# Optimization experiments

Measured on AMD Instinct MI355X. Metric: run time of the kernel, lower is better.

Reference implementation:

```python
import jax, jax.numpy as jnp
import numpy as np

N, L, D = 8, 2048, 128


def setup_inputs() -> dict:
    key = jax.random.key(0)
    k1, k2, k3, k4 = jax.random.split(key, 4)
    x_t = jax.random.normal(k1, (N, L, D), jnp.float32)
    x_f = jax.random.normal(k2, (N, L, D), jnp.float32)
    W = jax.random.normal(k3, (D, D), jnp.float32) / np.sqrt(D)  # proj weight (torch Linear layout)
    b = jax.random.normal(k4, (D,), jnp.float32) * 0.02
    return {"x_t": x_t, "x_f": x_f, "W": W, "b": b}


def _col_score(a, c, scale):
    # softmax attention with zeroed diagonal, then column-sum -> [N, L]
    att = jnp.einsum('nld,nmd->nlm', a, c) * scale
    att = jax.nn.softmax(att, axis=-1)
    att = att * (1.0 - jnp.eye(att.shape[-1], dtype=att.dtype))
    return jnp.sum(att, axis=1)


def _mask(score, time):
    # score: [N, L]; k-th extreme threshold, k = L//2
    k = int(0.5 * score.shape[1])
    if time:
        vals, _ = jax.lax.top_k(score, k)          # k largest, descending
        theta = vals[:, -1:]                        # k-th largest
        return score > theta
    else:
        vals, _ = jax.lax.top_k(-score, k)          # k smallest
        theta = -vals[:, -1:]                       # k-th smallest
        return score <= theta


def reference(x_t, x_f, W, b):
    scale = 1.0 / np.sqrt(W.shape[0])
    pt = x_t @ W.T + b
    pf = x_f @ W.T + b
    score_t = _col_score(pt, pt, scale)
    score_f = _col_score(pf, pf, scale)
    score_tf = _col_score(pt, pf, scale)
    score_ft = _col_score(pf, pt, scale)
    mask_t = _mask(score_t, False)
    mask_f = _mask(score_f, False)
    mask_tf = _mask(score_tf, True)   # computed in original forward (unused in blend)
    mask_ft = _mask(score_ft, True)
    mask_t1 = (mask_t & ~mask_f)[:, :, None]   # [N, L, 1] broadcast over D
    mask_f1 = (mask_f & ~mask_t)[:, :, None]
    x_t1 = jnp.where(mask_t1, x_f, x_t)
    x_f1 = jnp.where(mask_f1, x_t, x_f)
    return (0.5 * (x_t1 + x_t), 0.5 * (x_f1 + x_f))
```

## Files before the change

kernel.cpp:

```cpp
#include <hip/hip_runtime.h>
#include <math.h>

#define LL 2048
#define DD 128
#define NS 16
#define SLAB (LL * DD)
#define SCALE 0.08838834764831845f
#define NT 16
#define NPAIR 136
#define LSTR 40

typedef __attribute__((ext_vector_type(8))) short short8v;
typedef __attribute__((ext_vector_type(4))) float float4v;

__device__ __forceinline__ unsigned int f2bf(float f) {
    unsigned int u = __float_as_uint(f);
    u += 0x7fffu + ((u >> 16) & 1u);
    return u >> 16;
}
__device__ __forceinline__ void pair_decode(int p, int& ib, int& jb) {
    int i = 0;
    while (p >= NT - i) { p -= NT - i; ++i; }
    ib = i; jb = i + p;
}

__global__ __launch_bounds__(256, 4) void proj_kernel(
    const float* __restrict__ xt, const float* __restrict__ xf,
    const float* __restrict__ W,  const float* __restrict__ bias,
    unsigned short* __restrict__ Ph, unsigned short* __restrict__ Pl)
{
    __shared__ float Alds[64 * 36];
    __shared__ float Blds[128 * 36];
    __shared__ float bs[128];
    const int ns = blockIdx.y;
    const int l0 = blockIdx.x * 64;
    const int src = ns >> 3, n = ns & 7;
    const float* x = (src ? xf : xt) + (size_t)n * LL * DD;
    const int tid = threadIdx.x;
    const int ty = tid >> 4, tx = tid & 15;

    if (tid < 128) bs[tid] = bias[tid];
    __syncthreads();

    float acc[4][8];
#pragma unroll
    for (int i = 0; i < 4; ++i)
#pragma unroll
        for (int j = 0; j < 8; ++j) acc[i][j] = bs[tx + 16 * j];

    for (int kc = 0; kc < 4; ++kc) {
        __syncthreads();
#pragma unroll
        for (int t = 0; t < 2; ++t) {
            int idx = tid + t * 256;
            int r = idx >> 3, k4 = (idx & 7) << 2;
            *(float4*)&Alds[r * 36 + k4] =
                *(const float4*)&x[(size_t)(l0 + r) * DD + kc * 32 + k4];
        }
#pragma unroll
        for (int t = 0; t < 4; ++t) {
            int idx = tid + t * 256;
            int r = idx >> 3, k4 = (idx & 7) << 2;
            *(float4*)&Blds[r * 36 + k4] =
                *(const float4*)&W[(size_t)r * DD + kc * 32 + k4];
        }
        __syncthreads();
#pragma unroll
        for (int k4 = 0; k4 < 32; k4 += 4) {
            float4 a4[4], b4[8];
#pragma unroll
            for (int i = 0; i < 4; ++i) a4[i] = *(const float4*)&Alds[(ty + 16 * i) * 36 + k4];
#pragma unroll
            for (int j = 0; j < 8; ++j) b4[j] = *(const float4*)&Blds[(tx + 16 * j) * 36 + k4];
#pragma unroll
            for (int i = 0; i < 4; ++i)
#pragma unroll
                for (int j = 0; j < 8; ++j) {
                    acc[i][j] = fmaf(a4[i].x, b4[j].x, acc[i][j]);
                    acc[i][j] = fmaf(a4[i].y, b4[j].y, acc[i][j]);
                    acc[i][j] = fmaf(a4[i].z, b4[j].z, acc[i][j]);
                    acc[i][j] = fmaf(a4[i].w, b4[j].w, acc[i][j]);
                }
        }
    }
#pragma unroll
    for (int i = 0; i < 4; ++i) {
        const size_t rowo = (size_t)ns * SLAB + (size_t)(l0 + ty + 16 * i) * DD;
#pragma unroll
        for (int j = 0; j < 8; ++j) {
            float p = acc[i][j];
            unsigned int hb = f2bf(p);
            float hf = __uint_as_float(hb << 16);
            unsigned int lb = f2bf(p - hf);
            Ph[rowo + tx + 16 * j] = (unsigned short)hb;
            Pl[rowo + tx + 16 * j] = (unsigned short)lb;
        }
    }
}

__device__ __forceinline__ void mfma_core(
    const unsigned short* __restrict__ Ph, const unsigned short* __restrict__ Pl,
    int ns, int ib, int jb, int tid,
    unsigned short* Ah, unsigned short* Alo, unsigned short* Bh, unsigned short* Blo,
    float4v acc[2][8])
{
    const int lane = tid & 63;
    const int quad = lane >> 4, l16 = lane & 15;
    const int wave = tid >> 6;
    const int arow = wave * 32;
    const unsigned short* sAh = Ph + (size_t)ns * SLAB + (size_t)ib * 128 * DD;
    const unsigned short* sAl = Pl + (size_t)ns * SLAB + (size_t)ib * 128 * DD;
    const unsigned short* sBh = Ph + (size_t)ns * SLAB + (size_t)jb * 128 * DD;
    const unsigned short* sBl = Pl + (size_t)ns * SLAB + (size_t)jb * 128 * DD;

#pragma unroll
    for (int rt = 0; rt < 2; ++rt)
#pragma unroll
        for (int ct = 0; ct < 8; ++ct)
#pragma unroll
            for (int r = 0; r < 4; ++r) acc[rt][ct][r] = 0.f;

    for (int kc = 0; kc < 4; ++kc) {
        __syncthreads();
#pragma unroll
        for (int it = 0; it < 2; ++it) {
            int idx = tid + it * 256;
            int r = idx >> 2, c4 = idx & 3;
            size_t go = (size_t)r * DD + kc * 32 + c4 * 8;
            int lo = r * LSTR + c4 * 8;
            *(uint4*)&Ah[lo]  = *(const uint4*)&sAh[go];
            *(uint4*)&Alo[lo] = *(const uint4*)&sAl[go];
            *(uint4*)&Bh[lo]  = *(const uint4*)&sBh[go];
            *(uint4*)&Blo[lo] = *(const uint4*)&sBl[go];
        }
        __syncthreads();
        const int kb = quad * 8;
        short8v bh[8], bl[8];
#pragma unroll
        for (int ct = 0; ct < 8; ++ct) {
            int ba = (ct * 16 + l16) * LSTR + kb;
            bh[ct] = *(const short8v*)&Bh[ba];
            bl[ct] = *(const short8v*)&Blo[ba];
        }
#pragma unroll
        for (int rt = 0; rt < 2; ++rt) {
            int aa = (arow + rt * 16 + l16) * LSTR + kb;
            short8v ah = *(const short8v*)&Ah[aa];
            short8v al = *(const short8v*)&Alo[aa];
#pragma unroll
            for (int ct = 0; ct < 8; ++ct) {
                acc[rt][ct] = __builtin_amdgcn_mfma_f32_16x16x32_bf16(ah, bh[ct], acc[rt][ct], 0, 0, 0);
                acc[rt][ct] = __builtin_amdgcn_mfma_f32_16x16x32_bf16(ah, bl[ct], acc[rt][ct], 0, 0, 0);
                acc[rt][ct] = __builtin_amdgcn_mfma_f32_16x16x32_bf16(al, bh[ct], acc[rt][ct], 0, 0, 0);
            }
        }
    }
}

__global__ __launch_bounds__(256, 3) void stats_kernel(
    const unsigned short* __restrict__ Ph, const unsigned short* __restrict__ Pl,
    float* __restrict__ Zpart)
{
    __shared__ unsigned int AhU[2560], AlU[2560], BhU[2560], BlU[2560];
    int ib, jb;  pair_decode(blockIdx.x, ib, jb);
    const int ns = blockIdx.y;
    const int tid = threadIdx.x;
    const int lane = tid & 63, quad = lane >> 4, l16 = lane & 15, wave = tid >> 6;
    const int arow = wave * 32;

    float4v acc[2][8];
    mfma_core(Ph, Pl, ns, ib, jb, tid,
              (unsigned short*)AhU, (unsigned short*)AlU,
              (unsigned short*)BhU, (unsigned short*)BlU, acc);

    float cs[8];
#pragma unroll
    for (int ct = 0; ct < 8; ++ct) cs[ct] = 0.f;

#pragma unroll
    for (int rt = 0; rt < 2; ++rt)
#pragma unroll
        for (int rg = 0; rg < 4; ++rg) {
            float e[8];
#pragma unroll
            for (int ct = 0; ct < 8; ++ct) e[ct] = __expf(acc[rt][ct][rg] * SCALE);
            float s = 0.f;
#pragma unroll
            for (int ct = 0; ct < 8; ++ct) { s += e[ct]; cs[ct] += e[ct]; }
            s += __shfl_xor(s, 1);
            s += __shfl_xor(s, 2);
            s += __shfl_xor(s, 4);
            s += __shfl_xor(s, 8);
            if (l16 == 0) {
                int o = (ns * 16 + jb) * LL + ib * 128 + arow + rt * 16 + quad * 4 + rg;
                Zpart[o] = s;
            }
        }

    if (ib != jb) {
#pragma unroll
        for (int ct = 0; ct < 8; ++ct) {
            float s = cs[ct];
            s += __shfl_xor(s, 16);
            s += __shfl_xor(s, 32);
            cs[ct] = s;
        }
        __syncthreads();
        float* scs = (float*)AhU;
        if (quad == 0) {
#pragma unroll
            for (int ct = 0; ct < 8; ++ct) scs[(ct * 16 + l16) * 5 + wave] = cs[ct];
        }
        __syncthreads();
        if (tid < 128) {
            float S = scs[tid * 5] + scs[tid * 5 + 1] + scs[tid * 5 + 2] + scs[tid * 5 + 3];
            Zpart[(ns * 16 + ib) * LL + jb * 128 + tid] = S;
        }
    }
}

__global__ __launch_bounds__(256) void reduce_stats_kernel(
    const float* __restrict__ Zpart, float* __restrict__ iZfin)
{
    const int idx = blockIdx.x * 256 + threadIdx.x;
    const int ns = idx >> 11, l = idx & 2047;
    float Z = 0.f;
#pragma unroll
    for (int t = 0; t < 16; ++t) Z += Zpart[(ns * 16 + t) * LL + l];
    iZfin[idx] = 1.0f / Z;
}

__global__ __launch_bounds__(256, 3) void colsum_kernel(
    const unsigned short* __restrict__ Ph, const unsigned short* __restrict__ Pl,
    const float* __restrict__ iZfin, float* __restrict__ Spart)
{
    __shared__ unsigned int AhU[2560], AlU[2560], BhU[2560], BlU[2560];
    int ib, jb;  pair_decode(blockIdx.x, ib, jb);
    const int ns = blockIdx.y;
    const int tid = threadIdx.x;
    const int lane = tid & 63, quad = lane >> 4, l16 = lane & 15, wave = tid >> 6;
    const int arow = wave * 32;

    float4v acc[2][8];
    mfma_core(Ph, Pl, ns, ib, jb, tid,
              (unsigned short*)AhU, (unsigned short*)AlU,
              (unsigned short*)BhU, (unsigned short*)BlU, acc);

    float wrow[2][4];
#pragma unroll
    for (int rt = 0; rt < 2; ++rt)
#pragma unroll
        for (int rg = 0; rg < 4; ++rg)
            wrow[rt][rg] = iZfin[ns * LL + ib * 128 + arow + rt * 16 + quad * 4 + rg];
    float wcol[8];
#pragma unroll
    for (int ct = 0; ct < 8; ++ct)
        wcol[ct] = iZfin[ns * LL + jb * 128 + ct * 16 + l16];

    float dsum[8];
#pragma unroll
    for (int ct = 0; ct < 8; ++ct) dsum[ct] = 0.f;

#pragma unroll
    for (int rt = 0; rt < 2; ++rt)
#pragma unroll
        for (int rg = 0; rg < 4; ++rg) {
            const int rl = arow + rt * 16 + quad * 4 + rg;
            float ts = 0.f;
#pragma unroll
            for (int ct = 0; ct < 8; ++ct) {
                float e = __expf(acc[rt][ct][rg] * SCALE);
                bool diag = (ib == jb) && (rl == ct * 16 + l16);
                dsum[ct] += diag ? 0.f : e * wrow[rt][rg];
                ts += e * wcol[ct];
            }
            if (ib != jb) {
                ts += __shfl_xor(ts, 1);
                ts += __shfl_xor(ts, 2);
                ts += __shfl_xor(ts, 4);
                ts += __shfl_xor(ts, 8);
                if (l16 == 0)
                    Spart[((size_t)ns * LL + ib * 128 + rl) * 16 + jb] = ts;
            }
        }

#pragma unroll
    for (int ct = 0; ct < 8; ++ct) {
        float s = dsum[ct];
        s += __shfl_xor(s, 16);
        s += __shfl_xor(s, 32);
        dsum[ct] = s;
    }
    __syncthreads();
    float* scr = (float*)AhU;
    if (quad == 0) {
#pragma unroll
        for (int ct = 0; ct < 8; ++ct) scr[(ct * 16 + l16) * 5 + wave] = dsum[ct];
    }
    __syncthreads();
    if (tid < 128) {
        float t = scr[tid * 5] + scr[tid * 5 + 1] + scr[tid * 5 + 2] + scr[tid * 5 + 3];
        Spart[((size_t)ns * LL + jb * 128 + tid) * 16 + ib] = t;
    }
}

__global__ __launch_bounds__(1024) void mask_kernel(
    const float* __restrict__ Spart, unsigned char* __restrict__ maskbuf)
{
    __shared__ double s[LL];
    const int ns = blockIdx.x;
    const int half = blockIdx.y;
    const int tid = threadIdx.x;
#pragma unroll
    for (int h = 0; h < 2; ++h) {
        int m = tid + h * 1024;
        const float* sp = Spart + ((size_t)ns * LL + m) * 16;
        double a = 0.0;
#pragma unroll
        for (int t = 0; t < 16; ++t) a += (double)sp[t];
        s[m] = a;
    }
    __syncthreads();
    const int i = half * 1024 + tid;
    const double si = s[i];
    int cnt = 0;
    for (int j = 0; j < LL; ++j) cnt += (s[j] < si) ? 1 : 0;
    maskbuf[ns * LL + i] = (cnt < 1024) ? 1 : 0;
}

__global__ __launch_bounds__(256) void blend_kernel(
    const float* __restrict__ xt, const float* __restrict__ xf,
    const unsigned char* __restrict__ maskbuf, float* __restrict__ out)
{
    const int idx4 = blockIdx.x * 256 + threadIdx.x;
    const size_t q = (size_t)idx4 * 4;
    const int row = (int)(q >> 7);
    const float4 a = *(const float4*)(xt + q);
    const float4 b = *(const float4*)(xf + q);
    const int mt = maskbuf[row] & 1;
    const int mf = maskbuf[16384 + row] & 1;
    const bool ct = mt && !mf;
    const bool cf = mf && !mt;
    float4 av;
    av.x = 0.5f * (a.x + b.x);  av.y = 0.5f * (a.y + b.y);
    av.z = 0.5f * (a.z + b.z);  av.w = 0.5f * (a.w + b.w);
    float4 o0 = ct ? av : a;
    float4 o1 = cf ? av : b;
    *(float4*)(out + q)                   = o0;
    *(float4*)(out + (size_t)2097152 + q) = o1;
}

extern "C" void kernel_launch(void* const* d_in, const int* in_sizes, int n_in,
                              void* d_out, int out_size, void* d_ws, size_t ws_size,
                              hipStream_t stream)
{
    const float* xt = (const float*)d_in[0];
    const float* xf = (const float*)d_in[1];
    const float* W  = (const float*)d_in[2];
    const float* b  = (const float*)d_in[3];
    float* out = (float*)d_out;

    unsigned short* Ph = (unsigned short*)d_out;
    unsigned short* Pl = Ph + (size_t)NS * SLAB;

    float* Zpart = (float*)d_ws;
    float* iZfin = Zpart + 16 * 16 * LL;
    float* Spart = iZfin + NS * LL;
    unsigned char* maskbuf = (unsigned char*)(Spart + (size_t)16 * LL * 16);

    proj_kernel<<<dim3(32, NS), 256, 0, stream>>>(xt, xf, W, b, Ph, Pl);
    stats_kernel<<<dim3(NPAIR, NS), 256, 0, stream>>>(Ph, Pl, Zpart);
    reduce_stats_kernel<<<128, 256, 0, stream>>>(Zpart, iZfin);
    colsum_kernel<<<dim3(NPAIR, NS), 256, 0, stream>>>(Ph, Pl, iZfin, Spart);
    mask_kernel<<<dim3(NS, 2), 1024, 0, stream>>>(Spart, maskbuf);
    blend_kernel<<<2048, 256, 0, stream>>>(xt, xf, maskbuf, out);
}
```

Measured before the change: 225.7 us.

## Double-buffer B tiles via global_load_lds and use 2x2 wave tiling in MFMA core

Reworks the shared MFMA core. The B tile is now staged into double-buffered LDS with direct global-to-LDS loads, prefetching the next K chunk while the current one computes. The A operand is read straight from global memory into registers, and the four waves move from a 4x1 to a 2x2 arrangement with 64x64 tiles each. The epilogues switch to LDS partial arrays for the row and column reductions. The aim is to cut LDS traffic and barrier stalls and to hide load latency, at the cost of uncached global reads for A and some extra LDS for the reduction arrays.

```diff
diff --git a/kernel.cpp b/kernel.cpp
--- a/kernel.cpp
+++ b/kernel.cpp
@@ -8,7 +8,6 @@
 #define SCALE 0.08838834764831845f
 #define NT 16
 #define NPAIR 136
-#define LSTR 40
 
 typedef __attribute__((ext_vector_type(8))) short short8v;
 typedef __attribute__((ext_vector_type(4))) float float4v;
@@ -22,6 +21,23 @@
     int i = 0;
     while (p >= NT - i) { p -= NT - i; ++i; }
     ib = i; jb = i + p;
+}
+
+__device__ __forceinline__ void gl_lds16(const void* g, void* l) {
+    __builtin_amdgcn_global_load_lds(
+        (const __attribute__((address_space(1))) void*)g,
+        (__attribute__((address_space(3))) void*)l, 16, 0, 0);
+}
+
+__device__ __forceinline__ void stage_tile(
+    const unsigned short* __restrict__ gB, unsigned short* lbuf, int tid)
+{
+#pragma unroll
+    for (int it = 0; it < 2; ++it) {
+        const int c  = tid + it * 256;
+        const int cb = (tid & ~63) + it * 256;
+        gl_lds16(gB + (size_t)(c & 127) * DD + (c >> 7) * 8, lbuf + cb * 8);
+    }
 }
 
 __global__ __launch_bounds__(256, 4) void proj_kernel(
@@ -101,59 +117,68 @@
 __device__ __forceinline__ void mfma_core(
     const unsigned short* __restrict__ Ph, const unsigned short* __restrict__ Pl,
     int ns, int ib, int jb, int tid,
-    unsigned short* Ah, unsigned short* Alo, unsigned short* Bh, unsigned short* Blo,
-    float4v acc[2][8])
+    unsigned short* B0h, unsigned short* B1h,
+    unsigned short* B0l, unsigned short* B1l,
+    float4v (&acc)[4][4])
 {
     const int lane = tid & 63;
     const int quad = lane >> 4, l16 = lane & 15;
     const int wave = tid >> 6;
-    const int arow = wave * 32;
+    const int wr = wave >> 1, wc = wave & 1;
+
     const unsigned short* sAh = Ph + (size_t)ns * SLAB + (size_t)ib * 128 * DD;
     const unsigned short* sAl = Pl + (size_t)ns * SLAB + (size_t)ib * 128 * DD;
     const unsigned short* sBh = Ph + (size_t)ns * SLAB + (size_t)jb * 128 * DD;
     const unsigned short* sBl = Pl + (size_t)ns * SLAB + (size_t)jb * 128 * DD;
 
 #pragma unroll
-    for (int rt = 0; rt < 2; ++rt)
-#pragma unroll
-        for (int ct = 0; ct < 8; ++ct)
-#pragma unroll
-            for (int r = 0; r < 4; ++r) acc[rt][ct][r] = 0.f;
-
+    for (int i = 0; i < 4; ++i)
+#pragma unroll
+        for (int j = 0; j < 4; ++j)
+#pragma unroll
+            for (int r = 0; r < 4; ++r) acc[i][j][r] = 0.f;
+
+    unsigned short* bufh[2] = {B0h, B1h};
+    unsigned short* bufl[2] = {B0l, B1l};
+
+    stage_tile(sBh, bufh[0], tid);
+    stage_tile(sBl, bufl[0], tid);
+    __syncthreads();
+
+    const int arow0 = wr * 64;
+#pragma unroll
     for (int kc = 0; kc < 4; ++kc) {
+        short8v ah[4], al[4];
+        const int acol = kc * 32 + quad * 8;
+#pragma unroll
+        for (int rt = 0; rt < 4; ++rt) {
+            const size_t ao = (size_t)(arow0 + rt * 16 + l16) * DD + acol;
+            ah[rt] = *(const short8v*)&sAh[ao];
+            al[rt] = *(const short8v*)&sAl[ao];
+        }
+        __builtin_amdgcn_sched_barrier(0);
+        if (kc < 3) {
+            stage_tile(sBh + (kc + 1) * 32, bufh[(kc + 1) & 1], tid);
+            stage_tile(sBl + (kc + 1) * 32, bufl[(kc + 1) & 1], tid);
+        }
+        const unsigned short* bph = bufh[kc & 1];
+        const unsigned short* bpl = bufl[kc & 1];
+        short8v bh[4], bl[4];
+#pragma unroll
+        for (int ct = 0; ct < 4; ++ct) {
+            const int off = (quad * 128 + wc * 64 + ct * 16 + l16) * 8;
+            bh[ct] = *(const short8v*)&bph[off];
+            bl[ct] = *(const short8v*)&bpl[off];
+        }
+#pragma unroll
+        for (int rt = 0; rt < 4; ++rt)
+#pragma unroll
+            for (int ct = 0; ct < 4; ++ct) {
+                acc[rt][ct] = __builtin_amdgcn_mfma_f32_16x16x32_bf16(ah[rt], bh[ct], acc[rt][ct], 0, 0, 0);
+                acc[rt][ct] = __builtin_amdgcn_mfma_f32_16x16x32_bf16(ah[rt], bl[ct], acc[rt][ct], 0, 0, 0);
+                acc[rt][ct] = __builtin_amdgcn_mfma_f32_16x16x32_bf16(al[rt], bh[ct], acc[rt][ct], 0, 0, 0);
+            }
         __syncthreads();
-#pragma unroll
-        for (int it = 0; it < 2; ++it) {
-            int idx = tid + it * 256;
-            int r = idx >> 2, c4 = idx & 3;
-            size_t go = (size_t)r * DD + kc * 32 + c4 * 8;
-            int lo = r * LSTR + c4 * 8;
-            *(uint4*)&Ah[lo]  = *(const uint4*)&sAh[go];
-            *(uint4*)&Alo[lo] = *(const uint4*)&sAl[go];
-            *(uint4*)&Bh[lo]  = *(const uint4*)&sBh[go];
-            *(uint4*)&Blo[lo] = *(const uint4*)&sBl[go];
-        }
-        __syncthreads();
-        const int kb = quad * 8;
-        short8v bh[8], bl[8];
-#pragma unroll
-        for (int ct = 0; ct < 8; ++ct) {
-            int ba = (ct * 16 + l16) * LSTR + kb;
-            bh[ct] = *(const short8v*)&Bh[ba];
-            bl[ct] = *(const short8v*)&Blo[ba];
-        }
-#pragma unroll
-        for (int rt = 0; rt < 2; ++rt) {
-            int aa = (arow + rt * 16 + l16) * LSTR + kb;
-            short8v ah = *(const short8v*)&Ah[aa];
-            short8v al = *(const short8v*)&Alo[aa];
-#pragma unroll
-            for (int ct = 0; ct < 8; ++ct) {
-                acc[rt][ct] = __builtin_amdgcn_mfma_f32_16x16x32_bf16(ah, bh[ct], acc[rt][ct], 0, 0, 0);
-                acc[rt][ct] = __builtin_amdgcn_mfma_f32_16x16x32_bf16(ah, bl[ct], acc[rt][ct], 0, 0, 0);
-                acc[rt][ct] = __builtin_amdgcn_mfma_f32_16x16x32_bf16(al, bh[ct], acc[rt][ct], 0, 0, 0);
-            }
-        }
     }
 }
 
@@ -161,61 +186,48 @@
     const unsigned short* __restrict__ Ph, const unsigned short* __restrict__ Pl,
     float* __restrict__ Zpart)
 {
-    __shared__ unsigned int AhU[2560], AlU[2560], BhU[2560], BlU[2560];
+    __shared__ unsigned short B0h[4096], B1h[4096], B0l[4096], B1l[4096];
+    __shared__ float Zr[128][2], Zc[128][2];
     int ib, jb;  pair_decode(blockIdx.x, ib, jb);
     const int ns = blockIdx.y;
     const int tid = threadIdx.x;
     const int lane = tid & 63, quad = lane >> 4, l16 = lane & 15, wave = tid >> 6;
-    const int arow = wave * 32;
-
-    float4v acc[2][8];
-    mfma_core(Ph, Pl, ns, ib, jb, tid,
-              (unsigned short*)AhU, (unsigned short*)AlU,
-              (unsigned short*)BhU, (unsigned short*)BlU, acc);
-
-    float cs[8];
-#pragma unroll
-    for (int ct = 0; ct < 8; ++ct) cs[ct] = 0.f;
-
-#pragma unroll
-    for (int rt = 0; rt < 2; ++rt)
+    const int wr = wave >> 1, wc = wave & 1;
+
+    float4v acc[4][4];
+    mfma_core(Ph, Pl, ns, ib, jb, tid, B0h, B1h, B0l, B1l, acc);
+
+    float cs[4] = {0.f, 0.f, 0.f, 0.f};
+#pragma unroll
+    for (int rt = 0; rt < 4; ++rt)
 #pragma unroll
         for (int rg = 0; rg < 4; ++rg) {
-            float e[8];
-#pragma unroll
-            for (int ct = 0; ct < 8; ++ct) e[ct] = __expf(acc[rt][ct][rg] * SCALE);
+            float e[4];
             float s = 0.f;
 #pragma unroll
-            for (int ct = 0; ct < 8; ++ct) { s += e[ct]; cs[ct] += e[ct]; }
+            for (int ct = 0; ct < 4; ++ct) {
+                e[ct] = __expf(acc[rt][ct][rg] * SCALE);
+                s += e[ct]; cs[ct] += e[ct];
+            }
             s += __shfl_xor(s, 1);
             s += __shfl_xor(s, 2);
             s += __shfl_xor(s, 4);
             s += __shfl_xor(s, 8);
-            if (l16 == 0) {
-                int o = (ns * 16 + jb) * LL + ib * 128 + arow + rt * 16 + quad * 4 + rg;
-                Zpart[o] = s;
-            }
-        }
-
-    if (ib != jb) {
-#pragma unroll
-        for (int ct = 0; ct < 8; ++ct) {
-            float s = cs[ct];
-            s += __shfl_xor(s, 16);
-            s += __shfl_xor(s, 32);
-            cs[ct] = s;
-        }
-        __syncthreads();
-        float* scs = (float*)AhU;
-        if (quad == 0) {
-#pragma unroll
-            for (int ct = 0; ct < 8; ++ct) scs[(ct * 16 + l16) * 5 + wave] = cs[ct];
-        }
-        __syncthreads();
-        if (tid < 128) {
-            float S = scs[tid * 5] + scs[tid * 5 + 1] + scs[tid * 5 + 2] + scs[tid * 5 + 3];
-            Zpart[(ns * 16 + ib) * LL + jb * 128 + tid] = S;
-        }
+            if (l16 == 0) Zr[wr * 64 + rt * 16 + quad * 4 + rg][wc] = s;
+        }
+
+#pragma unroll
+    for (int ct = 0; ct < 4; ++ct) {
+        float s = cs[ct];
+        s += __shfl_xor(s, 16);
+        s += __shfl_xor(s, 32);
+        if (quad == 0) Zc[wc * 64 + ct * 16 + l16][wr] = s;
+    }
+    __syncthreads();
+    if (tid < 128) {
+        Zpart[(ns * 16 + jb) * LL + ib * 128 + tid] = Zr[tid][0] + Zr[tid][1];
+        if (ib != jb)
+            Zpart[(ns * 16 + ib) * LL + jb * 128 + tid] = Zc[tid][0] + Zc[tid][1];
     }
 }
 
@@ -234,43 +246,39 @@
     const unsigned short* __restrict__ Ph, const unsigned short* __restrict__ Pl,
     const float* __restrict__ iZfin, float* __restrict__ Spart)
 {
-    __shared__ unsigned int AhU[2560], AlU[2560], BhU[2560], BlU[2560];
+    __shared__ unsigned short B0h[4096], B1h[4096], B0l[4096], B1l[4096];
+    __shared__ float Sr[128][2], Sc[128][2];
     int ib, jb;  pair_decode(blockIdx.x, ib, jb);
     const int ns = blockIdx.y;
     const int tid = threadIdx.x;
     const int lane = tid & 63, quad = lane >> 4, l16 = lane & 15, wave = tid >> 6;
-    const int arow = wave * 32;
-
-    float4v acc[2][8];
-    mfma_core(Ph, Pl, ns, ib, jb, tid,
-              (unsigned short*)AhU, (unsigned short*)AlU,
-              (unsigned short*)BhU, (unsigned short*)BlU, acc);
-
-    float wrow[2][4];
-#pragma unroll
-    for (int rt = 0; rt < 2; ++rt)
+    const int wr = wave >> 1, wc = wave & 1;
+
+    float4v acc[4][4];
+    mfma_core(Ph, Pl, ns, ib, jb, tid, B0h, B1h, B0l, B1l, acc);
+
+    float wrow[4][4];
+#pragma unroll
+    for (int rt = 0; rt < 4; ++rt)
 #pragma unroll
         for (int rg = 0; rg < 4; ++rg)
-            wrow[rt][rg] = iZfin[ns * LL + ib * 128 + arow + rt * 16 + quad * 4 + rg];
-    float wcol[8];
-#pragma unroll
-    for (int ct = 0; ct < 8; ++ct)
-        wcol[ct] = iZfin[ns * LL + jb * 128 + ct * 16 + l16];
-
-    float dsum[8];
-#pragma unroll
-    for (int ct = 0; ct < 8; ++ct) dsum[ct] = 0.f;
-
-#pragma unroll
-    for (int rt = 0; rt < 2; ++rt)
+            wrow[rt][rg] = iZfin[ns * LL + ib * 128 + wr * 64 + rt * 16 + quad * 4 + rg];
+    float wcol[4];
+#pragma unroll
+    for (int ct = 0; ct < 4; ++ct)
+        wcol[ct] = iZfin[ns * LL + jb * 128 + wc * 64 + ct * 16 + l16];
+
+    float dsum[4] = {0.f, 0.f, 0.f, 0.f};
+#pragma unroll
+    for (int rt = 0; rt < 4; ++rt)
 #pragma unroll
         for (int rg = 0; rg < 4; ++rg) {
-            const int rl = arow + rt * 16 + quad * 4 + rg;
+            const int rl = wr * 64 + rt * 16 + quad * 4 + rg;
             float ts = 0.f;
 #pragma unroll
-            for (int ct = 0; ct < 8; ++ct) {
+            for (int ct = 0; ct < 4; ++ct) {
                 float e = __expf(acc[rt][ct][rg] * SCALE);
-                bool diag = (ib == jb) && (rl == ct * 16 + l16);
+                bool diag = (ib == jb) && (rl == wc * 64 + ct * 16 + l16);
                 dsum[ct] += diag ? 0.f : e * wrow[rt][rg];
                 ts += e * wcol[ct];
             }
@@ -279,28 +287,22 @@
                 ts += __shfl_xor(ts, 2);
                 ts += __shfl_xor(ts, 4);
                 ts += __shfl_xor(ts, 8);
-                if (l16 == 0)
-                    Spart[((size_t)ns * LL + ib * 128 + rl) * 16 + jb] = ts;
+                if (l16 == 0) Sr[rl][wc] = ts;
             }
         }
 
 #pragma unroll
-    for (int ct = 0; ct < 8; ++ct) {
+    for (int ct = 0; ct < 4; ++ct) {
         float s = dsum[ct];
         s += __shfl_xor(s, 16);
         s += __shfl_xor(s, 32);
-        dsum[ct] = s;
-    }
-    __syncthreads();
-    float* scr = (float*)AhU;
-    if (quad == 0) {
-#pragma unroll
-        for (int ct = 0; ct < 8; ++ct) scr[(ct * 16 + l16) * 5 + wave] = dsum[ct];
+        if (quad == 0) Sc[wc * 64 + ct * 16 + l16][wr] = s;
     }
     __syncthreads();
     if (tid < 128) {
-        float t = scr[tid * 5] + scr[tid * 5 + 1] + scr[tid * 5 + 2] + scr[tid * 5 + 3];
-        Spart[((size_t)ns * LL + jb * 128 + tid) * 16 + ib] = t;
+        Spart[((size_t)ns * LL + jb * 128 + tid) * 16 + ib] = Sc[tid][0] + Sc[tid][1];
+        if (ib != jb)
+            Spart[((size_t)ns * LL + ib * 128 + tid) * 16 + jb] = Sr[tid][0] + Sr[tid][1];
     }
 }
 
```

New measurement: 265.1 us. +17.5%, slower.
